# Kernel optimization log

Measured on AMD Instinct MI355X. Metric: run time of the kernel, lower is better.

The kernel has to match this reference:

```python
import jax, jax.numpy as jnp
import numpy as np

N_NODES = 100000
N_FEAT = 128
HID = 8
HEADS1 = 8
OUT2 = 32
NEG_SLOPE = 0.2


def gat_conv(x, W, a_src, a_dst, b, src, dst, n_nodes, concat):
    # x: [N, Fin], W: [Fin, H*C], a_src/a_dst: [H, C], b: [H*C] or [C]
    H, C = a_src.shape
    h = (x @ W).reshape(n_nodes, H, C)                      # [N, H, C]
    e_src = jnp.sum(h * a_src, axis=-1)                     # [N, H]
    e_dst = jnp.sum(h * a_dst, axis=-1)                     # [N, H]
    e = jax.nn.leaky_relu(e_src[src] + e_dst[dst], NEG_SLOPE)  # [E, H]
    m = jax.ops.segment_max(e, dst, num_segments=n_nodes)   # [N, H] (self-loops => no empty segment)
    ex = jnp.exp(e - m[dst])                                # [E, H]
    denom = jax.ops.segment_sum(ex, dst, num_segments=n_nodes)
    alpha = ex / denom[dst]                                 # [E, H]
    out = jax.ops.segment_sum(alpha[:, :, None] * h[src], dst, num_segments=n_nodes)  # [N, H, C]
    out = out.reshape(n_nodes, H * C) if concat else out.mean(axis=1)
    return out + b


def setup_inputs() -> dict:
    key = jax.random.key(0)
    ks = jax.random.split(key, 12)
    x = jax.random.normal(ks[0], (N_NODES, N_FEAT), dtype=jnp.float32)
    edge_index = jax.random.randint(ks[1], (2, 3200000), 0, N_NODES, dtype=jnp.int64)
    s1 = 1.0 / np.sqrt(N_FEAT)
    s2 = 1.0 / np.sqrt(HID * HEADS1)
    return {
        "x": x,
        "edge_index": edge_index,
        "W1": jax.random.normal(ks[2], (N_FEAT, HEADS1 * HID), dtype=jnp.float32) * s1,
        "a_src1": jax.random.normal(ks[3], (HEADS1, HID), dtype=jnp.float32) * s2,
        "a_dst1": jax.random.normal(ks[4], (HEADS1, HID), dtype=jnp.float32) * s2,
        "b1": jnp.zeros((HEADS1 * HID,), dtype=jnp.float32),
        "W2": jax.random.normal(ks[5], (HEADS1 * HID, OUT2), dtype=jnp.float32) * s2,
        "a_src2": jax.random.normal(ks[6], (1, OUT2), dtype=jnp.float32) * (1.0 / np.sqrt(OUT2)),
        "a_dst2": jax.random.normal(ks[7], (1, OUT2), dtype=jnp.float32) * (1.0 / np.sqrt(OUT2)),
        "b2": jnp.zeros((OUT2,), dtype=jnp.float32),
        "Wr": jax.random.normal(ks[8], (OUT2, 1), dtype=jnp.float32) * (1.0 / np.sqrt(OUT2)),
        "br": jnp.zeros((1,), dtype=jnp.float32),
    }


def reference(x, edge_index, W1, a_src1, a_dst1, b1, W2, a_src2, a_dst2, b2, Wr, br):
    n = x.shape[0]
    # PyG GATConv default add_self_loops=True
    loops = jnp.arange(n, dtype=edge_index.dtype)
    src = jnp.concatenate([edge_index[0], loops])
    dst = jnp.concatenate([edge_index[1], loops])
    h = gat_conv(x, W1, a_src1, a_dst1, b1, src, dst, n, concat=True)   # [N, 64]
    h = jax.nn.elu(h)
    h = gat_conv(h, W2, a_src2, a_dst2, b2, src, dst, n, concat=False)  # [N, 32]
    pooled = jnp.sum(h, axis=0, keepdims=True)                          # SumAggregation -> [1, 32]
    return pooled @ Wr + br                                             # [1, 1]
```

## Files before the change

kernel.cpp:

```cpp
#include <hip/hip_runtime.h>
#include <math.h>

#define NEG_SLOPE 0.2f
#define FIN 128
#define H1 8
#define F1 64
#define F2 32

#define SHIFT 5
#define BW 32
#define CAPL 2048
#define CAP_G 1408
#define NBMAX 4096

typedef unsigned short ushort_t;
typedef unsigned int uint_t;

#define LO16(u) __uint_as_float((u) << 16)
#define HI16(u) __uint_as_float((u) & 0xffff0000u)

static __device__ __forceinline__ ushort_t f2bf(float f) {
    uint_t u = __float_as_uint(f);
    u = (u + 0x7FFFu + ((u >> 16) & 1u)) >> 16;
    return (ushort_t)u;
}
static __device__ __forceinline__ float bf2f(ushort_t h) {
    return __uint_as_float(((uint_t)h) << 16);
}
static __device__ __forceinline__ uint_t packAB(float e) {
    return (uint_t)f2bf(__expf(e)) | ((uint_t)f2bf(__expf(NEG_SLOPE * e)) << 16);
}

__global__ void gemm1_kernel(const float* __restrict__ x, const float* __restrict__ W1,
                             const float* __restrict__ a_src, const float* __restrict__ a_dst,
                             ushort_t* __restrict__ h1, uint_t* __restrict__ sp,
                             float* __restrict__ ed, int N) {
    __shared__ float xs[16][FIN];
    int tid = threadIdx.x;
    int n0 = blockIdx.x * 16;
    for (int i = tid; i < 16 * FIN; i += 256) {
        int nn = n0 + (i >> 7);
        xs[i >> 7][i & 127] = (nn < N) ? x[(size_t)nn * FIN + (i & 127)] : 0.f;
    }
    __syncthreads();
    int wv = tid >> 6, j = tid & 63;
    int nb = wv << 2;
    float a0 = 0.f, a1 = 0.f, a2 = 0.f, a3 = 0.f;
#pragma unroll 2
    for (int k = 0; k < FIN; k += 4) {
        float w0 = W1[(k + 0) * F1 + j];
        float w1 = W1[(k + 1) * F1 + j];
        float w2 = W1[(k + 2) * F1 + j];
        float w3 = W1[(k + 3) * F1 + j];
        float4 x0 = *(const float4*)&xs[nb + 0][k];
        float4 x1 = *(const float4*)&xs[nb + 1][k];
        float4 x2 = *(const float4*)&xs[nb + 2][k];
        float4 x3 = *(const float4*)&xs[nb + 3][k];
        a0 = fmaf(x0.x, w0, fmaf(x0.y, w1, fmaf(x0.z, w2, fmaf(x0.w, w3, a0))));
        a1 = fmaf(x1.x, w0, fmaf(x1.y, w1, fmaf(x1.z, w2, fmaf(x1.w, w3, a1))));
        a2 = fmaf(x2.x, w0, fmaf(x2.y, w1, fmaf(x2.z, w2, fmaf(x2.w, w3, a2))));
        a3 = fmaf(x3.x, w0, fmaf(x3.y, w1, fmaf(x3.z, w2, fmaf(x3.w, w3, a3))));
    }
    float as = a_src[j], ad = a_dst[j];
    float av[4] = {a0, a1, a2, a3};
#pragma unroll
    for (int t = 0; t < 4; ++t) {
        int n = n0 + nb + t;
        if (n >= N) break;
        h1[(size_t)n * F1 + j] = f2bf(av[t]);
        float vs = av[t] * as;
        float vd = av[t] * ad;
#pragma unroll
        for (int off = 4; off >= 1; off >>= 1) {
            vs += __shfl_down(vs, off, 8);
            vd += __shfl_down(vd, off, 8);
        }
        if ((j & 7) == 0) {
            sp[n * H1 + (j >> 3)] = packAB(vs);
            ed[n * H1 + (j >> 3)] = vd;
        }
    }
}

__global__ void zerob_kernel(int* __restrict__ bcnt, int* __restrict__ boff,
                             int NB, float* __restrict__ pooled, int capg) {
    int t = blockIdx.x * blockDim.x + threadIdx.x;
    int stride = gridDim.x * blockDim.x;
    for (int i = t; i < NB; i += stride) {
        bcnt[i] = 0;
        if (capg) boff[i] = i * capg;
    }
    if (t == 0 && blockIdx.x == 0) pooled[0] = 0.f;
}

__global__ void bscat_static(const int* __restrict__ ei, int E, int N,
                             int* __restrict__ bcnt, const int* __restrict__ boff,
                             uint_t* __restrict__ pk) {
    __shared__ int lh[NBMAX];
    __shared__ int lc[NBMAX];
    int tid = threadIdx.x;
    int NB = (N + BW - 1) >> SHIFT;
    for (int i = tid; i < NB; i += 256) lh[i] = 0;
    __syncthreads();
    int EN = E + N;
    int chunk = (EN + gridDim.x - 1) / gridDim.x;
    int e0 = blockIdx.x * chunk;
    int e1 = e0 + chunk; if (e1 > EN) e1 = EN;
    for (int t = e0 + tid; t < e1; t += 256) {
        int d = (t < E) ? ei[E + t] : (t - E);
        atomicAdd(&lh[d >> SHIFT], 1);
    }
    __syncthreads();
    for (int i = tid; i < NB; i += 256) {
        int c = lh[i];
        lc[i] = c ? (boff[i] + atomicAdd(&bcnt[i], c)) : 0;
    }
    __syncthreads();
    for (int t = e0 + tid; t < e1; t += 256) {
        int s, d;
        if (t < E) { s = ei[t]; d = ei[E + t]; } else { s = d = t - E; }
        int pos = atomicAdd(&lc[d >> SHIFT], 1);
        pk[pos] = ((uint_t)s << SHIFT) | (uint_t)(d & (BW - 1));
    }
}

__global__ void bhist_kernel(const int* __restrict__ ei, int E, int N,
                             int* __restrict__ bcnt, int NB) {
    __shared__ int h[NBMAX];
    int tid = threadIdx.x;
    for (int i = tid; i < NB; i += 256) h[i] = 0;
    __syncthreads();
    int EN = E + N;
    int chunk = (EN + gridDim.x - 1) / gridDim.x;
    int e0 = blockIdx.x * chunk;
    int e1 = e0 + chunk; if (e1 > EN) e1 = EN;
    for (int t = e0 + tid; t < e1; t += 256) {
        int d = (t < E) ? ei[E + t] : (t - E);
        atomicAdd(&h[d >> SHIFT], 1);
    }
    __syncthreads();
    for (int i = tid; i < NB; i += 256)
        if (h[i]) atomicAdd(&bcnt[i], h[i]);
}

__global__ void bscan_kernel(const int* __restrict__ bcnt, int NB,
                             int* __restrict__ boff, int* __restrict__ bcur) {
    int lane = threadIdx.x;
    int chunk = (NB + 63) >> 6;
    int lo = lane * chunk;
    int hi = lo + chunk; if (hi > NB) hi = NB;
    int sum = 0;
    for (int i = lo; i < hi; ++i) sum += bcnt[i];
    int e = sum;
#pragma unroll
    for (int o = 1; o < 64; o <<= 1) {
        int v = __shfl_up(e, o, 64);
        if (lane >= o) e += v;
    }
    e -= sum;
    int run = e;
    for (int i = lo; i < hi; ++i) {
        int c = bcnt[i];
        boff[i] = run;
        bcur[i] = run;
        run += c;
    }
}

__global__ void bscat_kernel(const int* __restrict__ ei, int E, int N,
                             int* __restrict__ bcur, uint_t* __restrict__ pk, int NB) {
    __shared__ int lh[NBMAX];
    __shared__ int lc[NBMAX];
    int tid = threadIdx.x;
    for (int i = tid; i < NB; i += 256) lh[i] = 0;
    __syncthreads();
    int EN = E + N;
    int chunk = (EN + gridDim.x - 1) / gridDim.x;
    int e0 = blockIdx.x * chunk;
    int e1 = e0 + chunk; if (e1 > EN) e1 = EN;
    for (int t = e0 + tid; t < e1; t += 256) {
        int d = (t < E) ? ei[E + t] : (t - E);
        atomicAdd(&lh[d >> SHIFT], 1);
    }
    __syncthreads();
    for (int i = tid; i < NB; i += 256) {
        int c = lh[i];
        lc[i] = c ? atomicAdd(&bcur[i], c) : 0;
    }
    __syncthreads();
    for (int t = e0 + tid; t < e1; t += 256) {
        int s, d;
        if (t < E) { s = ei[t]; d = ei[E + t]; } else { s = d = t - E; }
        int pos = atomicAdd(&lc[d >> SHIFT], 1);
        pk[pos] = ((uint_t)s << SHIFT) | (uint_t)(d & (BW - 1));
    }
}

__global__ void __launch_bounds__(256, 8)
edge1_gather(const int* __restrict__ bcnt, const int* __restrict__ boff,
             const uint_t* __restrict__ pk,
             const uint_t* __restrict__ sp, const float* __restrict__ ed,
             const ushort_t* __restrict__ h1, float* __restrict__ o1, int N) {
    int b = blockIdx.x;
    int d0 = b << SHIFT;
    int cnt = bcnt[b];
    int gbase = boff[b];
    int tid = threadIdx.x;
    int wv = tid >> 6;
    int L = tid & 63;
    int q = L >> 4;
    int c4 = (L & 15) << 2;
    int hL = (L & 15) >> 1;
    __shared__ int ldeg[BW];
    __shared__ int loff[BW];
    __shared__ int lcur[BW];
    __shared__ int lsrc[CAPL];
    if (cnt <= CAPL) {
        if (tid < BW) ldeg[tid] = 0;
        __syncthreads();
        for (int k = tid; k < cnt; k += 256) atomicAdd(&ldeg[pk[gbase + k] & (BW - 1)], 1);
        __syncthreads();
        if (tid < BW) {
            int v = ldeg[tid];
            int e = v;
#pragma unroll
            for (int o = 1; o < BW; o <<= 1) {
                int u = __shfl_up(e, o, 64);
                if (tid >= o) e += u;
            }
            e -= v;
            loff[tid] = e;
            lcur[tid] = e;
        }
        __syncthreads();
        for (int k = tid; k < cnt; k += 256) {
            uint_t v = pk[gbase + k];
            int pos = atomicAdd(&lcur[v & (BW - 1)], 1);
            lsrc[pos] = (int)(v >> SHIFT);
        }
        __syncthreads();
        for (int ld = wv * 8; ld < wv * 8 + 8; ++ld) {
            int d = d0 + ld;
            if (d >= N) break;
            int st = loff[ld], en = st + ldeg[ld];
            float edv = ed[d * H1 + hL];
            float Ad = __expf(edv), Bd = __expf(NEG_SLOPE * edv);
            float ax = 0.f, ay = 0.f, az = 0.f, aw = 0.f, wsum = 0.f;
            uint_t U0, U1; uint2 V0, V1;
            {
                int i0 = st + q, i1 = st + 4 + q;
                bool ok0 = i0 < en, ok1 = i1 < en;
                int s0 = lsrc[ok0 ? i0 : st];
                int s1 = lsrc[ok1 ? i1 : st];
                uint_t u0 = sp[s0 * H1 + hL];
                uint_t u1 = sp[s1 * H1 + hL];
                V0 = *(const uint2*)(h1 + ((size_t)s0 << 6) + c4);
                V1 = *(const uint2*)(h1 + ((size_t)s1 << 6) + c4);
                U0 = ok0 ? u0 : 0u;
                U1 = ok1 ? u1 : 0u;
            }
            for (int k = st; k < en; k += 8) {
                uint_t N0, N1; uint2 P0, P1;
                {
                    int i0 = k + 8 + q, i1 = k + 12 + q;
                    bool ok0 = i0 < en, ok1 = i1 < en;
                    int s0 = lsrc[ok0 ? i0 : st];
                    int s1 = lsrc[ok1 ? i1 : st];
                    uint_t u0 = sp[s0 * H1 + hL];
                    uint_t u1 = sp[s1 * H1 + hL];
                    P0 = *(const uint2*)(h1 + ((size_t)s0 << 6) + c4);
                    P1 = *(const uint2*)(h1 + ((size_t)s1 << 6) + c4);
                    N0 = ok0 ? u0 : 0u;
                    N1 = ok1 ? u1 : 0u;
                }
                float w0 = fmaxf(LO16(U0) * Ad, HI16(U0) * Bd);
                float w1 = fmaxf(LO16(U1) * Ad, HI16(U1) * Bd);
                ax = fmaf(w0, LO16(V0.x), ax);
                ay = fmaf(w0, HI16(V0.x), ay);
                az = fmaf(w0, LO16(V0.y), az);
                aw = fmaf(w0, HI16(V0.y), aw);
                ax = fmaf(w1, LO16(V1.x), ax);
                ay = fmaf(w1, HI16(V1.x), ay);
                az = fmaf(w1, LO16(V1.y), az);
                aw = fmaf(w1, HI16(V1.y), aw);
                wsum += w0 + w1;
                U0 = N0; U1 = N1; V0 = P0; V1 = P1;
            }
            ax += __shfl_xor(ax, 16, 64); ax += __shfl_xor(ax, 32, 64);
            ay += __shfl_xor(ay, 16, 64); ay += __shfl_xor(ay, 32, 64);
            az += __shfl_xor(az, 16, 64); az += __shfl_xor(az, 32, 64);
            aw += __shfl_xor(aw, 16, 64); aw += __shfl_xor(aw, 32, 64);
            wsum += __shfl_xor(wsum, 16, 64); wsum += __shfl_xor(wsum, 32, 64);
            if (q == 0) {
                float inv = 1.f / wsum;
                float4 r; r.x = ax * inv; r.y = ay * inv; r.z = az * inv; r.w = aw * inv;
                *(float4*)(o1 + (size_t)d * F1 + c4) = r;
            }
        }
    } else {
        for (int ld = wv * 8; ld < wv * 8 + 8; ++ld) {
            int d = d0 + ld;
            if (d >= N) break;
            float edv = ed[d * H1 + hL];
            float Ad = __expf(edv), Bd = __expf(NEG_SLOPE * edv);
            float ax = 0.f, ay = 0.f, az = 0.f, aw = 0.f, wsum = 0.f;
            for (int k0 = 0; k0 < cnt; k0 += 4) {
                int idx = k0 + q;
                bool ok = idx < cnt;
                uint_t v = pk[gbase + (ok ? idx : 0)];
                int s = (int)(v >> SHIFT);
                bool m = ok && ((int)(v & (BW - 1)) == ld);
                uint_t u = sp[(uint_t)s * H1 + hL];
                float w = m ? fmaxf(LO16(u) * Ad, HI16(u) * Bd) : 0.f;
                uint2 hv = *(const uint2*)(h1 + ((size_t)s << 6) + c4);
                ax = fmaf(w, LO16(hv.x), ax);
                ay = fmaf(w, HI16(hv.x), ay);
                az = fmaf(w, LO16(hv.y), az);
                aw = fmaf(w, HI16(hv.y), aw);
                wsum += w;
            }
            ax += __shfl_xor(ax, 16, 64); ax += __shfl_xor(ax, 32, 64);
            ay += __shfl_xor(ay, 16, 64); ay += __shfl_xor(ay, 32, 64);
            az += __shfl_xor(az, 16, 64); az += __shfl_xor(az, 32, 64);
            aw += __shfl_xor(aw, 16, 64); aw += __shfl_xor(aw, 32, 64);
            wsum += __shfl_xor(wsum, 16, 64); wsum += __shfl_xor(wsum, 32, 64);
            if (q == 0) {
                float inv = 1.f / wsum;
                float4 r; r.x = ax * inv; r.y = ay * inv; r.z = az * inv; r.w = aw * inv;
                *(float4*)(o1 + (size_t)d * F1 + c4) = r;
            }
        }
    }
}

__global__ void gemm2_kernel(const float* __restrict__ o1, const float* __restrict__ b1,
                             const float* __restrict__ W2,
                             const float* __restrict__ a_src2, const float* __restrict__ a_dst2,
                             ushort_t* __restrict__ h2, uint_t* __restrict__ sp2,
                             float* __restrict__ ed2, int N) {
    int half = threadIdx.x >> 5;
    int n = blockIdx.x * 8 + half;
    int j = threadIdx.x & 31;
    __shared__ float a1s[8][F1];
    if (n < N) {
#pragma unroll
        for (int r = 0; r < 2; ++r) {
            int k = r * 32 + j;
            float v = o1[(size_t)n * F1 + k] + b1[k];
            a1s[half][k] = v > 0.f ? v : expm1f(v);
        }
    }
    __syncthreads();
    if (n >= N) return;
    float acc = 0.f;
#pragma unroll
    for (int k = 0; k < F1; ++k) acc = fmaf(a1s[half][k], W2[k * F2 + j], acc);
    h2[(size_t)n * F2 + j] = f2bf(acc);
    float vs = acc * a_src2[j];
    float vd = acc * a_dst2[j];
#pragma unroll
    for (int off = 16; off >= 1; off >>= 1) {
        vs += __shfl_down(vs, off, 32);
        vd += __shfl_down(vd, off, 32);
    }
    if (j == 0) {
        sp2[n] = packAB(vs);
        ed2[n] = vd;
    }
}

__global__ void __launch_bounds__(256, 8)
edge2_gather(const int* __restrict__ bcnt, const int* __restrict__ boff,
             const uint_t* __restrict__ pk,
             const uint_t* __restrict__ sp2, const float* __restrict__ ed2,
             const ushort_t* __restrict__ h2,
             const float* __restrict__ b2, const float* __restrict__ Wr,
             float* __restrict__ pooled, int N) {
    int b = blockIdx.x;
    int d0 = b << SHIFT;
    int cnt = bcnt[b];
    int gbase = boff[b];
    int tid = threadIdx.x;
    int wv = tid >> 6;
    int L = tid & 63;
    int q = L >> 4;
    int cc = (L & 15) << 1;
    __shared__ int ldeg[BW];
    __shared__ int loff[BW];
    __shared__ int lcur[BW];
    __shared__ int lsrc[CAPL];
    float wr0 = Wr[cc], wr1 = Wr[cc + 1];
    float b2w = b2[cc] * wr0 + b2[cc + 1] * wr1;
    float part = 0.f;
    if (cnt <= CAPL) {
        if (tid < BW) ldeg[tid] = 0;
        __syncthreads();
        for (int k = tid; k < cnt; k += 256) atomicAdd(&ldeg[pk[gbase + k] & (BW - 1)], 1);
        __syncthreads();
        if (tid < BW) {
            int v = ldeg[tid];
            int e = v;
#pragma unroll
            for (int o = 1; o < BW; o <<= 1) {
                int u = __shfl_up(e, o, 64);
                if (tid >= o) e += u;
            }
            e -= v;
            loff[tid] = e;
            lcur[tid] = e;
        }
        __syncthreads();
        for (int k = tid; k < cnt; k += 256) {
            uint_t v = pk[gbase + k];
            int pos = atomicAdd(&lcur[v & (BW - 1)], 1);
            lsrc[pos] = (int)(v >> SHIFT);
        }
        __syncthreads();
        for (int ld = wv * 8; ld < wv * 8 + 8; ++ld) {
            int d = d0 + ld;
            if (d >= N) break;
            int st = loff[ld], en = st + ldeg[ld];
            float edv = ed2[d];
            float Ad = __expf(edv), Bd = __expf(NEG_SLOPE * edv);
            float a0 = 0.f, a1 = 0.f, wsum = 0.f;
            uint_t U0, U1, V0, V1;
            {
                int i0 = st + q, i1 = st + 4 + q;
                bool ok0 = i0 < en, ok1 = i1 < en;
                int s0 = lsrc[ok0 ? i0 : st];
                int s1 = lsrc[ok1 ? i1 : st];
                uint_t u0 = sp2[s0];
                uint_t u1 = sp2[s1];
                V0 = *(const uint_t*)(h2 + (size_t)s0 * F2 + cc);
                V1 = *(const uint_t*)(h2 + (size_t)s1 * F2 + cc);
                U0 = ok0 ? u0 : 0u;
                U1 = ok1 ? u1 : 0u;
            }
            for (int k = st; k < en; k += 8) {
                uint_t N0, N1, P0, P1;
                {
                    int i0 = k + 8 + q, i1 = k + 12 + q;
                    bool ok0 = i0 < en, ok1 = i1 < en;
                    int s0 = lsrc[ok0 ? i0 : st];
                    int s1 = lsrc[ok1 ? i1 : st];
                    uint_t u0 = sp2[s0];
                    uint_t u1 = sp2[s1];
                    P0 = *(const uint_t*)(h2 + (size_t)s0 * F2 + cc);
                    P1 = *(const uint_t*)(h2 + (size_t)s1 * F2 + cc);
                    N0 = ok0 ? u0 : 0u;
                    N1 = ok1 ? u1 : 0u;
                }
                float w0 = fmaxf(LO16(U0) * Ad, HI16(U0) * Bd);
                float w1 = fmaxf(LO16(U1) * Ad, HI16(U1) * Bd);
                a0 = fmaf(w0, LO16(V0), a0);
                a1 = fmaf(w0, HI16(V0), a1);
                a0 = fmaf(w1, LO16(V1), a0);
                a1 = fmaf(w1, HI16(V1), a1);
                wsum += w0 + w1;
                U0 = N0; U1 = N1; V0 = P0; V1 = P1;
            }
            a0 += __shfl_xor(a0, 16, 64); a0 += __shfl_xor(a0, 32, 64);
            a1 += __shfl_xor(a1, 16, 64); a1 += __shfl_xor(a1, 32, 64);
            wsum += __shfl_xor(wsum, 16, 64); wsum += __shfl_xor(wsum, 32, 64);
            if (q == 0) {
                float inv = 1.f / wsum;
                part += (a0 * wr0 + a1 * wr1) * inv + b2w;
            }
        }
    } else {
        for (int ld = wv * 8; ld < wv * 8 + 8; ++ld) {
            int d = d0 + ld;
            if (d >= N) break;
            float edv = ed2[d];
            float Ad = __expf(edv), Bd = __expf(NEG_SLOPE * edv);
            float a0 = 0.f, a1 = 0.f, wsum = 0.f;
            for (int k0 = 0; k0 < cnt; k0 += 4) {
                int idx = k0 + q;
                bool ok = idx < cnt;
                uint_t v = pk[gbase + (ok ? idx : 0)];
                int s = (int)(v >> SHIFT);
                bool m = ok && ((int)(v & (BW - 1)) == ld);
                uint_t u = m ? sp2[s] : 0u;
                uint_t hv = *(const uint_t*)(h2 + (size_t)s * F2 + cc);
                float w = fmaxf(LO16(u) * Ad, HI16(u) * Bd);
                a0 = fmaf(w, LO16(hv), a0);
                a1 = fmaf(w, HI16(hv), a1);
                wsum += w;
            }
            a0 += __shfl_xor(a0, 16, 64); a0 += __shfl_xor(a0, 32, 64);
            a1 += __shfl_xor(a1, 16, 64); a1 += __shfl_xor(a1, 32, 64);
            wsum += __shfl_xor(wsum, 16, 64); wsum += __shfl_xor(wsum, 32, 64);
            if (q == 0) {
                float inv = 1.f / wsum;
                part += (a0 * wr0 + a1 * wr1) * inv + b2w;
            }
        }
    }
#pragma unroll
    for (int o = 32; o >= 1; o >>= 1) part += __shfl_down(part, o, 64);
    __shared__ float ls[4];
    if ((tid & 63) == 0) ls[wv] = part;
    __syncthreads();
    if (tid == 0) atomicAdd(pooled, ls[0] + ls[1] + ls[2] + ls[3]);
}

__global__ void final_kernel(const float* __restrict__ pooled, const float* __restrict__ br,
                             float* __restrict__ out) {
    if (threadIdx.x == 0 && blockIdx.x == 0) out[0] = pooled[0] + br[0];
}

extern "C" void kernel_launch(void* const* d_in, const int* in_sizes, int n_in,
                              void* d_out, int out_size, void* d_ws, size_t ws_size,
                              hipStream_t stream) {
    const float* x    = (const float*)d_in[0];
    const int*   ei   = (const int*)d_in[1];
    const float* W1   = (const float*)d_in[2];
    const float* a_s1 = (const float*)d_in[3];
    const float* a_d1 = (const float*)d_in[4];
    const float* b1   = (const float*)d_in[5];
    const float* W2   = (const float*)d_in[6];
    const float* a_s2 = (const float*)d_in[7];
    const float* a_d2 = (const float*)d_in[8];
    const float* b2   = (const float*)d_in[9];
    const float* Wr   = (const float*)d_in[10];
    const float* br   = (const float*)d_in[11];
    float* out = (float*)d_out;

    int N = in_sizes[0] / FIN;
    int E = in_sizes[1] / 2;
    size_t n = (size_t)N;
    int NB = (N + BW - 1) >> SHIFT;

    char* ws = (char*)d_ws;
    float*    o1   = (float*)ws;
    uint_t*   sp1  = (uint_t*)(ws + n * 256);
    float*    ed1  = (float*)(ws + n * 288);
    ushort_t* h1   = (ushort_t*)(ws + n * 320);
    uint_t*   pk   = (uint_t*)(ws + n * 448);
    size_t pk_static = (size_t)NB * CAP_G * 4;
    size_t pk_exact  = (size_t)(E + N) * 4;
    bool use_static = ws_size >= n * 448 + pk_static + (size_t)NBMAX * 16 + 256;
    char* tail = ws + n * 448 + (use_static ? pk_static : pk_exact);
    int*      bcnt = (int*)tail;
    int*      boff = (int*)(tail + NBMAX * 4);
    int*      bcur = (int*)(tail + NBMAX * 8);
    float*  pooled = (float*)(tail + NBMAX * 12);
    ushort_t* h2  = h1;
    uint_t*   sp2 = sp1;
    float*    ed2 = ed1;

    zerob_kernel<<<8, 256, 0, stream>>>(bcnt, boff, NB, pooled, use_static ? CAP_G : 0);
    gemm1_kernel<<<(N + 15) / 16, 256, 0, stream>>>(x, W1, a_s1, a_d1, h1, sp1, ed1, N);
    if (use_static) {
        bscat_static<<<256, 256, 0, stream>>>(ei, E, N, bcnt, boff, pk);
    } else {
        bhist_kernel<<<256, 256, 0, stream>>>(ei, E, N, bcnt, NB);
        bscan_kernel<<<1, 64, 0, stream>>>(bcnt, NB, boff, bcur);
        bscat_kernel<<<256, 256, 0, stream>>>(ei, E, N, bcur, pk, NB);
    }
    edge1_gather<<<NB, 256, 0, stream>>>(bcnt, boff, pk, sp1, ed1, h1, o1, N);
    gemm2_kernel<<<(N + 7) / 8, 256, 0, stream>>>(o1, b1, W2, a_s2, a_d2, h2, sp2, ed2, N);
    edge2_gather<<<NB, 256, 0, stream>>>(bcnt, boff, pk, sp2, ed2, h2, b2, Wr, pooled, N);
    final_kernel<<<1, 64, 0, stream>>>(pooled, br, out);
}
```

Before: 437.9 us.

## Fuse gemm1 and static bucket scatter into one heterogeneous kernel launch

Merges the first-layer GEMM and the edge bucket scatter into a single launch. The first G2 blocks do the scatter and the remaining blocks do the GEMM, so the two independent stages run concurrently and one launch is saved. Scatter blocks now each handle 1024 edges, four per thread with int4 vector loads, instead of 256 blocks each striding over large chunks. The price is far more global atomicAdd calls on bcnt because there are many more blocks, plus mixed block types sharing one launch-bounds and LDS configuration.

```diff
diff --git a/kernel.cpp b/kernel.cpp
--- a/kernel.cpp
+++ b/kernel.cpp
@@ -29,6 +29,106 @@
 }
 static __device__ __forceinline__ uint_t packAB(float e) {
     return (uint_t)f2bf(__expf(e)) | ((uint_t)f2bf(__expf(NEG_SLOPE * e)) << 16);
+}
+
+__global__ void __launch_bounds__(256, 6)
+fused1_kernel(const float* __restrict__ x, const float* __restrict__ W1,
+              const float* __restrict__ a_src, const float* __restrict__ a_dst,
+              ushort_t* __restrict__ h1, uint_t* __restrict__ sp,
+              float* __restrict__ ed,
+              const int* __restrict__ ei, int* __restrict__ bcnt,
+              const int* __restrict__ boff, uint_t* __restrict__ pk,
+              int N, int E, int G2) {
+    __shared__ int sm[NBMAX];
+    int tid = threadIdx.x;
+    if ((int)blockIdx.x < G2) {
+        int NB = (N + BW - 1) >> SHIFT;
+        for (int i = tid; i < NB; i += 256) sm[i] = 0;
+        __syncthreads();
+        int EN = E + N;
+        int t0 = blockIdx.x * 1024 + tid * 4;
+        int s[4], d[4];
+        if (t0 + 4 <= E) {
+            int4 sv = *(const int4*)&ei[t0];
+            s[0] = sv.x; s[1] = sv.y; s[2] = sv.z; s[3] = sv.w;
+            if ((E & 3) == 0) {
+                int4 dv = *(const int4*)&ei[E + t0];
+                d[0] = dv.x; d[1] = dv.y; d[2] = dv.z; d[3] = dv.w;
+            } else {
+#pragma unroll
+                for (int r = 0; r < 4; ++r) d[r] = ei[E + t0 + r];
+            }
+        } else {
+#pragma unroll
+            for (int r = 0; r < 4; ++r) {
+                int t = t0 + r;
+                if (t < EN) {
+                    if (t < E) { s[r] = ei[t]; d[r] = ei[E + t]; }
+                    else       { s[r] = d[r] = t - E; }
+                } else d[r] = -1;
+            }
+        }
+#pragma unroll
+        for (int r = 0; r < 4; ++r)
+            if (d[r] >= 0) atomicAdd(&sm[d[r] >> SHIFT], 1);
+        __syncthreads();
+        for (int i = tid; i < NB; i += 256) {
+            int c = sm[i];
+            if (c) sm[i] = boff[i] + atomicAdd(&bcnt[i], c);
+        }
+        __syncthreads();
+#pragma unroll
+        for (int r = 0; r < 4; ++r)
+            if (d[r] >= 0) {
+                int pos = atomicAdd(&sm[d[r] >> SHIFT], 1);
+                pk[pos] = ((uint_t)s[r] << SHIFT) | (uint_t)(d[r] & (BW - 1));
+            }
+    } else {
+        float (*xs)[FIN] = (float (*)[FIN])sm;
+        int n0 = ((int)blockIdx.x - G2) * 16;
+        for (int i = tid; i < 16 * FIN; i += 256) {
+            int nn = n0 + (i >> 7);
+            xs[i >> 7][i & 127] = (nn < N) ? x[(size_t)nn * FIN + (i & 127)] : 0.f;
+        }
+        __syncthreads();
+        int wv = tid >> 6, j = tid & 63;
+        int nb = wv << 2;
+        float a0 = 0.f, a1 = 0.f, a2 = 0.f, a3 = 0.f;
+#pragma unroll 2
+        for (int k = 0; k < FIN; k += 4) {
+            float w0 = W1[(k + 0) * F1 + j];
+            float w1 = W1[(k + 1) * F1 + j];
+            float w2 = W1[(k + 2) * F1 + j];
+            float w3 = W1[(k + 3) * F1 + j];
+            float4 x0 = *(const float4*)&xs[nb + 0][k];
+            float4 x1 = *(const float4*)&xs[nb + 1][k];
+            float4 x2 = *(const float4*)&xs[nb + 2][k];
+            float4 x3 = *(const float4*)&xs[nb + 3][k];
+            a0 = fmaf(x0.x, w0, fmaf(x0.y, w1, fmaf(x0.z, w2, fmaf(x0.w, w3, a0))));
+            a1 = fmaf(x1.x, w0, fmaf(x1.y, w1, fmaf(x1.z, w2, fmaf(x1.w, w3, a1))));
+            a2 = fmaf(x2.x, w0, fmaf(x2.y, w1, fmaf(x2.z, w2, fmaf(x2.w, w3, a2))));
+            a3 = fmaf(x3.x, w0, fmaf(x3.y, w1, fmaf(x3.z, w2, fmaf(x3.w, w3, a3))));
+        }
+        float as = a_src[j], ad = a_dst[j];
+        float av[4] = {a0, a1, a2, a3};
+#pragma unroll
+        for (int t = 0; t < 4; ++t) {
+            int n = n0 + nb + t;
+            if (n >= N) break;
+            h1[(size_t)n * F1 + j] = f2bf(av[t]);
+            float vs = av[t] * as;
+            float vd = av[t] * ad;
+#pragma unroll
+            for (int off = 4; off >= 1; off >>= 1) {
+                vs += __shfl_down(vs, off, 8);
+                vd += __shfl_down(vd, off, 8);
+            }
+            if ((j & 7) == 0) {
+                sp[n * H1 + (j >> 3)] = packAB(vs);
+                ed[n * H1 + (j >> 3)] = vd;
+            }
+        }
+    }
 }
 
 __global__ void gemm1_kernel(const float* __restrict__ x, const float* __restrict__ W1,
@@ -91,37 +191,6 @@
         if (capg) boff[i] = i * capg;
     }
     if (t == 0 && blockIdx.x == 0) pooled[0] = 0.f;
-}
-
-__global__ void bscat_static(const int* __restrict__ ei, int E, int N,
-                             int* __restrict__ bcnt, const int* __restrict__ boff,
-                             uint_t* __restrict__ pk) {
-    __shared__ int lh[NBMAX];
-    __shared__ int lc[NBMAX];
-    int tid = threadIdx.x;
-    int NB = (N + BW - 1) >> SHIFT;
-    for (int i = tid; i < NB; i += 256) lh[i] = 0;
-    __syncthreads();
-    int EN = E + N;
-    int chunk = (EN + gridDim.x - 1) / gridDim.x;
-    int e0 = blockIdx.x * chunk;
-    int e1 = e0 + chunk; if (e1 > EN) e1 = EN;
-    for (int t = e0 + tid; t < e1; t += 256) {
-        int d = (t < E) ? ei[E + t] : (t - E);
-        atomicAdd(&lh[d >> SHIFT], 1);
-    }
-    __syncthreads();
-    for (int i = tid; i < NB; i += 256) {
-        int c = lh[i];
-        lc[i] = c ? (boff[i] + atomicAdd(&bcnt[i], c)) : 0;
-    }
-    __syncthreads();
-    for (int t = e0 + tid; t < e1; t += 256) {
-        int s, d;
-        if (t < E) { s = ei[t]; d = ei[E + t]; } else { s = d = t - E; }
-        int pos = atomicAdd(&lc[d >> SHIFT], 1);
-        pk[pos] = ((uint_t)s << SHIFT) | (uint_t)(d & (BW - 1));
-    }
 }
 
 __global__ void bhist_kernel(const int* __restrict__ ei, int E, int N,
@@ -550,10 +619,13 @@
     float*    ed2 = ed1;
 
     zerob_kernel<<<8, 256, 0, stream>>>(bcnt, boff, NB, pooled, use_static ? CAP_G : 0);
-    gemm1_kernel<<<(N + 15) / 16, 256, 0, stream>>>(x, W1, a_s1, a_d1, h1, sp1, ed1, N);
     if (use_static) {
-        bscat_static<<<256, 256, 0, stream>>>(ei, E, N, bcnt, boff, pk);
+        int G1 = (N + 15) / 16;
+        int G2 = (E + N + 1023) >> 10;
+        fused1_kernel<<<G1 + G2, 256, 0, stream>>>(x, W1, a_s1, a_d1, h1, sp1, ed1,
+                                                   ei, bcnt, boff, pk, N, E, G2);
     } else {
+        gemm1_kernel<<<(N + 15) / 16, 256, 0, stream>>>(x, W1, a_s1, a_d1, h1, sp1, ed1, N);
         bhist_kernel<<<256, 256, 0, stream>>>(ei, E, N, bcnt, NB);
         bscan_kernel<<<1, 64, 0, stream>>>(bcnt, NB, boff, bcur);
         bscat_kernel<<<256, 256, 0, stream>>>(ei, E, N, bcur, pk, NB);
```

After: 485.7 us. 1.11x slower.

## Replace single-pass bucket scatter with two-level radix partition of edges

Applied to the files above, without the earlier changes.

The one-pass scatter of edges into 32-node destination buckets is replaced by a two-pass partition. The first pass bins edges into 2048-node super-buckets using shared-memory staging and block-contiguous writes. The second pass sub-bins each super-bucket into the fine buckets with locally coalesced writes. The aim is to cut scattered global writes and global atomics on thousands of buckets. In exchange it adds an extra read and write pass over the edge list. It also reuses the o1 workspace as temporary storage, which is why gemm1 is now launched after partitioning.

```diff
diff --git a/kernel.cpp b/kernel.cpp
--- a/kernel.cpp
+++ b/kernel.cpp
@@ -12,6 +12,12 @@
 #define CAPL 2048
 #define CAP_G 1408
 #define NBMAX 4096
+
+#define SB_SHIFT 11
+#define NSBMAX 64
+#define P_CHUNK 2048
+#define BPS 35
+#define SBCAP (BPS * P_CHUNK)
 
 typedef unsigned short ushort_t;
 typedef unsigned int uint_t;
@@ -83,44 +89,150 @@
 }
 
 __global__ void zerob_kernel(int* __restrict__ bcnt, int* __restrict__ boff,
-                             int NB, float* __restrict__ pooled, int capg) {
+                             int NB, float* __restrict__ pooled, int capg,
+                             int* __restrict__ sbcnt, int nsb) {
     int t = blockIdx.x * blockDim.x + threadIdx.x;
     int stride = gridDim.x * blockDim.x;
     for (int i = t; i < NB; i += stride) {
         bcnt[i] = 0;
         if (capg) boff[i] = i * capg;
     }
-    if (t == 0 && blockIdx.x == 0) pooled[0] = 0.f;
-}
-
-__global__ void bscat_static(const int* __restrict__ ei, int E, int N,
-                             int* __restrict__ bcnt, const int* __restrict__ boff,
-                             uint_t* __restrict__ pk) {
-    __shared__ int lh[NBMAX];
-    __shared__ int lc[NBMAX];
+    for (int i = t; i < nsb; i += stride) sbcnt[i] = 0;
+    if (t == 0) pooled[0] = 0.f;
+}
+
+__global__ void __launch_bounds__(256, 4)
+part1_kernel(const int* __restrict__ ei, int E, int N,
+             int* __restrict__ sbcnt, uint_t* __restrict__ sbdata) {
+    __shared__ int hist[NSBMAX];
+    __shared__ int loff[NSBMAX];
+    __shared__ int lcur[NSBMAX];
+    __shared__ int gb[NSBMAX];
+    __shared__ uint_t buf[P_CHUNK];
+    __shared__ unsigned char sbarr[P_CHUNK];
     int tid = threadIdx.x;
-    int NB = (N + BW - 1) >> SHIFT;
-    for (int i = tid; i < NB; i += 256) lh[i] = 0;
+    int NSB = (N + ((1 << SB_SHIFT) - 1)) >> SB_SHIFT;
+    for (int i = tid; i < NSB; i += 256) hist[i] = 0;
     __syncthreads();
     int EN = E + N;
-    int chunk = (EN + gridDim.x - 1) / gridDim.x;
-    int e0 = blockIdx.x * chunk;
-    int e1 = e0 + chunk; if (e1 > EN) e1 = EN;
-    for (int t = e0 + tid; t < e1; t += 256) {
-        int d = (t < E) ? ei[E + t] : (t - E);
-        atomicAdd(&lh[d >> SHIFT], 1);
-    }
-    __syncthreads();
-    for (int i = tid; i < NB; i += 256) {
-        int c = lh[i];
-        lc[i] = c ? (boff[i] + atomicAdd(&bcnt[i], c)) : 0;
-    }
-    __syncthreads();
-    for (int t = e0 + tid; t < e1; t += 256) {
-        int s, d;
-        if (t < E) { s = ei[t]; d = ei[E + t]; } else { s = d = t - E; }
-        int pos = atomicAdd(&lc[d >> SHIFT], 1);
-        pk[pos] = ((uint_t)s << SHIFT) | (uint_t)(d & (BW - 1));
+    int base = blockIdx.x * P_CHUNK;
+    int m = EN - base; if (m > P_CHUNK) m = P_CHUNK;
+    int t0 = base + tid * 8;
+    int s[8], d[8];
+    bool fast = (t0 + 8 <= E) && ((E & 3) == 0);
+    if (fast) {
+        int4 a = *(const int4*)&ei[t0];
+        int4 b = *(const int4*)&ei[t0 + 4];
+        s[0]=a.x; s[1]=a.y; s[2]=a.z; s[3]=a.w; s[4]=b.x; s[5]=b.y; s[6]=b.z; s[7]=b.w;
+        int4 c = *(const int4*)&ei[E + t0];
+        int4 e2 = *(const int4*)&ei[E + t0 + 4];
+        d[0]=c.x; d[1]=c.y; d[2]=c.z; d[3]=c.w; d[4]=e2.x; d[5]=e2.y; d[6]=e2.z; d[7]=e2.w;
+    } else {
+#pragma unroll
+        for (int r = 0; r < 8; ++r) {
+            int t = t0 + r;
+            if (t < EN) {
+                if (t < E) { s[r] = ei[t]; d[r] = ei[E + t]; }
+                else       { s[r] = d[r] = t - E; }
+            } else d[r] = -1;
+        }
+    }
+#pragma unroll
+    for (int r = 0; r < 8; ++r)
+        if (d[r] >= 0) atomicAdd(&hist[d[r] >> SB_SHIFT], 1);
+    __syncthreads();
+    if (tid < 64) {
+        int v = (tid < NSB) ? hist[tid] : 0;
+        int e = v;
+#pragma unroll
+        for (int o = 1; o < 64; o <<= 1) {
+            int u = __shfl_up(e, o, 64);
+            if (tid >= o) e += u;
+        }
+        e -= v;
+        if (tid < NSB) {
+            loff[tid] = e;
+            lcur[tid] = e;
+            gb[tid] = v ? atomicAdd(&sbcnt[tid], v) : 0;
+        }
+    }
+    __syncthreads();
+#pragma unroll
+    for (int r = 0; r < 8; ++r)
+        if (d[r] >= 0) {
+            int sb = d[r] >> SB_SHIFT;
+            int pos = atomicAdd(&lcur[sb], 1);
+            buf[pos] = ((uint_t)s[r] << SB_SHIFT) | (uint_t)(d[r] & ((1 << SB_SHIFT) - 1));
+            sbarr[pos] = (unsigned char)sb;
+        }
+    __syncthreads();
+    for (int i = tid; i < m; i += 256) {
+        int sb = sbarr[i];
+        int idx = gb[sb] + (i - loff[sb]);
+        if (idx < SBCAP)
+            sbdata[(size_t)sb * SBCAP + idx] = buf[i];
+    }
+}
+
+__global__ void __launch_bounds__(256, 4)
+part2_kernel(const uint_t* __restrict__ sbdata, const int* __restrict__ sbcnt,
+             int* __restrict__ bcnt, const int* __restrict__ boff,
+             uint_t* __restrict__ pk) {
+    __shared__ int hist[64];
+    __shared__ int loff[64];
+    __shared__ int lcur[64];
+    __shared__ int gb[64];
+    __shared__ uint_t buf[P_CHUNK];
+    int tid = threadIdx.x;
+    int sb = blockIdx.x / BPS;
+    int base = (blockIdx.x % BPS) * P_CHUNK;
+    int cnt = sbcnt[sb];
+    if (cnt > SBCAP) cnt = SBCAP;
+    if (base >= cnt) return;
+    int m = cnt - base; if (m > P_CHUNK) m = P_CHUNK;
+    if (tid < 64) hist[tid] = 0;
+    __syncthreads();
+    const uint_t* src = sbdata + (size_t)sb * SBCAP + base;
+    uint_t v[8];
+#pragma unroll
+    for (int r = 0; r < 8; ++r) {
+        int i = tid + r * 256;
+        if (i < m) {
+            v[r] = src[i];
+            atomicAdd(&hist[(v[r] >> 5) & 63], 1);
+        }
+    }
+    __syncthreads();
+    if (tid < 64) {
+        int c = hist[tid];
+        int e = c;
+#pragma unroll
+        for (int o = 1; o < 64; o <<= 1) {
+            int u = __shfl_up(e, o, 64);
+            if (tid >= o) e += u;
+        }
+        e -= c;
+        loff[tid] = e;
+        lcur[tid] = e;
+        int bucket = (sb << 6) + tid;
+        gb[tid] = c ? (boff[bucket] + atomicAdd(&bcnt[bucket], c)) : 0;
+    }
+    __syncthreads();
+#pragma unroll
+    for (int r = 0; r < 8; ++r) {
+        int i = tid + r * 256;
+        if (i < m) {
+            int lb = (v[r] >> 5) & 63;
+            int pos = atomicAdd(&lcur[lb], 1);
+            buf[pos] = v[r];
+        }
+    }
+    __syncthreads();
+    for (int i = tid; i < m; i += 256) {
+        uint_t u = buf[i];
+        int lb = (u >> 5) & 63;
+        int idx = gb[lb] + (i - loff[lb]);
+        pk[idx] = ((u >> SB_SHIFT) << SHIFT) | (u & (BW - 1));
     }
 }
 
@@ -530,6 +642,7 @@
     int E = in_sizes[1] / 2;
     size_t n = (size_t)N;
     int NB = (N + BW - 1) >> SHIFT;
+    int NSB = (N + ((1 << SB_SHIFT) - 1)) >> SB_SHIFT;
 
     char* ws = (char*)d_ws;
     float*    o1   = (float*)ws;
@@ -539,21 +652,30 @@
     uint_t*   pk   = (uint_t*)(ws + n * 448);
     size_t pk_static = (size_t)NB * CAP_G * 4;
     size_t pk_exact  = (size_t)(E + N) * 4;
-    bool use_static = ws_size >= n * 448 + pk_static + (size_t)NBMAX * 16 + 256;
+    uint_t* sbdata = (uint_t*)ws;
+    bool use_static = (NSB <= NSBMAX) &&
+                      ((size_t)NSB * SBCAP * 4 <= n * 256) &&
+                      (ws_size >= n * 448 + pk_static + (size_t)NBMAX * 16 + NSBMAX * 4 + 256);
     char* tail = ws + n * 448 + (use_static ? pk_static : pk_exact);
-    int*      bcnt = (int*)tail;
-    int*      boff = (int*)(tail + NBMAX * 4);
-    int*      bcur = (int*)(tail + NBMAX * 8);
-    float*  pooled = (float*)(tail + NBMAX * 12);
+    int*      bcnt  = (int*)tail;
+    int*      boff  = (int*)(tail + NBMAX * 4);
+    int*      bcur  = (int*)(tail + NBMAX * 8);
+    int*      sbcnt = (int*)(tail + NBMAX * 12);
+    float*  pooled  = (float*)(tail + NBMAX * 12 + NSBMAX * 4);
     ushort_t* h2  = h1;
     uint_t*   sp2 = sp1;
     float*    ed2 = ed1;
 
-    zerob_kernel<<<8, 256, 0, stream>>>(bcnt, boff, NB, pooled, use_static ? CAP_G : 0);
-    gemm1_kernel<<<(N + 15) / 16, 256, 0, stream>>>(x, W1, a_s1, a_d1, h1, sp1, ed1, N);
+    zerob_kernel<<<8, 256, 0, stream>>>(bcnt, boff, NB, pooled,
+                                        use_static ? CAP_G : 0, sbcnt, NSB);
     if (use_static) {
-        bscat_static<<<256, 256, 0, stream>>>(ei, E, N, bcnt, boff, pk);
+        int EN = E + N;
+        int G1 = (EN + P_CHUNK - 1) / P_CHUNK;
+        part1_kernel<<<G1, 256, 0, stream>>>(ei, E, N, sbcnt, sbdata);
+        part2_kernel<<<NSB * BPS, 256, 0, stream>>>(sbdata, sbcnt, bcnt, boff, pk);
+        gemm1_kernel<<<(N + 15) / 16, 256, 0, stream>>>(x, W1, a_s1, a_d1, h1, sp1, ed1, N);
     } else {
+        gemm1_kernel<<<(N + 15) / 16, 256, 0, stream>>>(x, W1, a_s1, a_d1, h1, sp1, ed1, N);
         bhist_kernel<<<256, 256, 0, stream>>>(ei, E, N, bcnt, NB);
         bscan_kernel<<<1, 64, 0, stream>>>(bcnt, NB, boff, bcur);
         bscat_kernel<<<256, 256, 0, stream>>>(ei, E, N, bcur, pk, NB);
```

Measured after the change: 394.2 us. -10.0%, faster.
